# Kernel tuning notes

Measured on AMD Instinct MI355X. Metric: run time of the kernel, lower is better.

Reference implementation:

```python
import jax, jax.numpy as jnp
import numpy as np

E, T, D_IN, D_H = 8, 2048, 2048, 5632


def setup_inputs() -> dict:
    key = jax.random.key(0)
    kx, kg, kd, ku = jax.random.split(key, 4)
    scale = 0.02  # init_std-like scaling for weights
    return {
        "x": jax.random.normal(kx, (E, T, D_IN), dtype=jnp.float32),
        "gate_proj": jax.random.normal(kg, (E, D_IN, D_H), dtype=jnp.float32) * scale,
        "down_proj": jax.random.normal(kd, (E, D_IN, D_H), dtype=jnp.float32) * scale,
        "up_proj": jax.random.normal(ku, (E, D_H, D_IN), dtype=jnp.float32) * scale,
        "tokens_per_expert": T,
    }


def reference(x, gate_proj, down_proj, up_proj, tokens_per_expert):
    # ep_size=1: dispatch/combine are identity. Grouped SwiGLU per expert.
    # x: [E, T, d_in]; gate/down: [E, d_in, d_h]; up: [E, d_h, d_in]
    g = jnp.einsum('etd,edh->eth', x, gate_proj)
    u = jnp.einsum('etd,edh->eth', x, down_proj)
    h = jax.nn.silu(g) * u  # [E, T, d_h]
    out = jnp.einsum('eth,ehd->etd', h, up_proj)  # [E, T, d_in]
    return out
```

## Files before the change

### kernel.cpp

```cpp
#include <hip/hip_runtime.h>
#include <hip/hip_bf16.h>


#define NEXP 8
#define TT   2048
#define DIN  2048
#define DH   5632
#define KP   2080

using short8 = __attribute__((ext_vector_type(8))) short;
using f32x4  = __attribute__((ext_vector_type(4))) float;

static __device__ __forceinline__ unsigned short f2bf(float f) {
    unsigned int i = __float_as_uint(f);
    return (unsigned short)((i + 0x7FFFu + ((i >> 16) & 1u)) >> 16);
}
static __device__ __forceinline__ void gld16(const void* g, void* l) {
    __builtin_amdgcn_global_load_lds(
        (const __attribute__((address_space(1))) void*)g,
        (__attribute__((address_space(3))) void*)l, 16, 0, 0);
}

__global__ __launch_bounds__(512, 2) void gemm_gu(
    const unsigned short* __restrict__ Xb,
    const unsigned short* __restrict__ Wgt,
    const unsigned short* __restrict__ Wdt,
    unsigned short* __restrict__ Hb)
{
    __shared__ __align__(16) unsigned short lds[81920];

    const int tid  = threadIdx.x;
    const int wave = tid >> 6, lane = tid & 63;
    const int l15 = lane & 15, l4 = lane >> 4;
    const int wr = wave >> 2, wc = wave & 3;

    const int bid = blockIdx.x;
    const int e   = bid & 7;
    const int cu  = bid >> 3;
    const int m0  = (cu & 7) * 256;
    const int nb  = cu >> 3;

    const unsigned short* Ae = Xb + (size_t)e * TT * KP;
    unsigned short* He = Hb + (size_t)e * TT * DH;

    const int c0 = tid, c1 = 512 + tid;
    const int cs0 = c0 ^ ((c0 >> 3) & 7), cs1 = c1 ^ ((c1 >> 3) & 7);
    const int row0 = cs0 >> 3, col0 = (cs0 & 7) * 8;
    const int row1 = cs1 >> 3, col1 = (cs1 & 7) * 8;

    int ibA[4][2], ibB[2][2];
#pragma unroll
    for (int s = 0; s < 4; ++s)
#pragma unroll
        for (int ks = 0; ks < 2; ++ks) {
            const int r = wr * 64 + s * 16 + l15;
            ibA[s][ks] = (r * 128 + ks * 64 + l4 * 16) ^ ((r & 7) << 4);
        }
#pragma unroll
    for (int s = 0; s < 2; ++s)
#pragma unroll
        for (int ks = 0; ks < 2; ++ks) {
            const int r = wc * 32 + s * 16 + l15;
            ibB[s][ks] = (r * 128 + ks * 64 + l4 * 16) ^ ((r & 7) << 4);
        }

    f32x4 acc[8][4] = {};
    short8 Aq[4][2], Gq[2][2], Dq[2][2];

    char* ldsb = (char*)lds;
    auto stageA = [&](int ro, int kk, int so) {
        gld16(Ae + (size_t)(m0 + ro + row0) * KP + (kk + col0), ldsb + so + wave * 1024);
        gld16(Ae + (size_t)(m0 + ro + row1) * KP + (kk + col1), ldsb + so + 8192 + wave * 1024);
    };
    auto stageW = [&](const unsigned short* p, int kk, int so) {
        gld16(p + (size_t)row0 * KP + (kk + col0), ldsb + so + wave * 1024);
        gld16(p + (size_t)row1 * KP + (kk + col1), ldsb + so + 8192 + wave * 1024);
    };
    auto w10 = [](int x) { return x >= 10 ? x - 10 : x; };

    const size_t NSTEP = (size_t)512 * KP;
    const unsigned short* Gc = Wgt + (size_t)e * DH * KP + (size_t)(nb * 128) * KP;
    const unsigned short* Dc = Wdt + (size_t)e * DH * KP + (size_t)(nb * 128) * KP;

    stageA(0, 0, 0 << 14);  stageW(Gc, 0, 1 << 14);  stageW(Dc, 0, 2 << 14);  stageA(128, 0, 3 << 14);
    stageA(0, 64, 4 << 14); stageW(Gc, 64, 5 << 14); stageW(Dc, 64, 6 << 14);
    asm volatile("s_waitcnt vmcnt(6)" ::: "memory");
    asm volatile("s_barrier" ::: "memory");

    const char* ldsc = (const char*)lds;
    int q = 0;
    for (int i = 0; i < 11; ++i) {
        const unsigned short* Gn = Gc + NSTEP;
        const unsigned short* Dn = Dc + NSTEP;
        for (int t = 0; t < 32; ++t) {
            const int g = (i << 5) + t;
            const int sA0 = q << 14;
            const int sG  = w10(q + 1) << 14;
            const int sD  = w10(q + 2) << 14;
            const int sA1 = w10(q + 3) << 14;
            const int stA1 = w10(q + 7) << 14;
            const int stA0 = w10(q + 8) << 14;
            const int stG  = w10(q + 9) << 14;
            const int stD  = sA0;

#pragma unroll
            for (int s = 0; s < 4; ++s) {
                Aq[s][0] = *(const short8*)(ldsc + sA0 + ibA[s][0]);
                Aq[s][1] = *(const short8*)(ldsc + sA0 + ibA[s][1]);
            }
#pragma unroll
            for (int s = 0; s < 2; ++s) {
                Gq[s][0] = *(const short8*)(ldsc + sG + ibB[s][0]);
                Gq[s][1] = *(const short8*)(ldsc + sG + ibB[s][1]);
                Dq[s][0] = *(const short8*)(ldsc + sD + ibB[s][0]);
                Dq[s][1] = *(const short8*)(ldsc + sD + ibB[s][1]);
            }
            if (i < 10 || t + 1 < 32)
                stageA(128, ((t + 1) & 31) * 64, stA1);
            asm volatile("s_waitcnt lgkmcnt(0)" ::: "memory");
            __builtin_amdgcn_sched_barrier(0);
            __builtin_amdgcn_s_setprio(1);
#pragma unroll
            for (int m = 0; m < 4; ++m)
#pragma unroll
                for (int n = 0; n < 2; ++n) {
                    acc[m][n] = __builtin_amdgcn_mfma_f32_16x16x32_bf16(Aq[m][0], Gq[n][0], acc[m][n], 0, 0, 0);
                    acc[m][n] = __builtin_amdgcn_mfma_f32_16x16x32_bf16(Aq[m][1], Gq[n][1], acc[m][n], 0, 0, 0);
                }
            __builtin_amdgcn_s_setprio(0);
            if (i < 10 || t + 2 < 32)
                stageA(0, ((t + 2) & 31) * 64, stA0);
            __builtin_amdgcn_s_setprio(1);
#pragma unroll
            for (int m = 0; m < 4; ++m)
#pragma unroll
                for (int n = 0; n < 2; ++n) {
                    acc[m][2 + n] = __builtin_amdgcn_mfma_f32_16x16x32_bf16(Aq[m][0], Dq[n][0], acc[m][2 + n], 0, 0, 0);
                    acc[m][2 + n] = __builtin_amdgcn_mfma_f32_16x16x32_bf16(Aq[m][1], Dq[n][1], acc[m][2 + n], 0, 0, 0);
                }
            __builtin_amdgcn_s_setprio(0);
#pragma unroll
            for (int s = 0; s < 4; ++s) {
                Aq[s][0] = *(const short8*)(ldsc + sA1 + ibA[s][0]);
                Aq[s][1] = *(const short8*)(ldsc + sA1 + ibA[s][1]);
            }
            if (i < 10 || t + 2 < 32)
                stageW((t + 2 < 32) ? Gc : Gn, ((t + 2) & 31) * 64, stG);
            asm volatile("s_waitcnt lgkmcnt(0)" ::: "memory");
            __builtin_amdgcn_sched_barrier(0);
            __builtin_amdgcn_s_setprio(1);
#pragma unroll
            for (int m = 0; m < 4; ++m)
#pragma unroll
                for (int n = 0; n < 2; ++n) {
                    acc[4 + m][2 + n] = __builtin_amdgcn_mfma_f32_16x16x32_bf16(Aq[m][0], Dq[n][0], acc[4 + m][2 + n], 0, 0, 0);
                    acc[4 + m][2 + n] = __builtin_amdgcn_mfma_f32_16x16x32_bf16(Aq[m][1], Dq[n][1], acc[4 + m][2 + n], 0, 0, 0);
                }
#pragma unroll
            for (int m = 0; m < 4; ++m)
#pragma unroll
                for (int n = 0; n < 2; ++n) {
                    acc[4 + m][n] = __builtin_amdgcn_mfma_f32_16x16x32_bf16(Aq[m][0], Gq[n][0], acc[4 + m][n], 0, 0, 0);
                    acc[4 + m][n] = __builtin_amdgcn_mfma_f32_16x16x32_bf16(Aq[m][1], Gq[n][1], acc[4 + m][n], 0, 0, 0);
                }
            __builtin_amdgcn_s_setprio(0);
            asm volatile("s_barrier" ::: "memory");
            if (i < 10 || t + 2 < 32)
                stageW((t + 2 < 32) ? Dc : Dn, ((t + 2) & 31) * 64, stD);
            if (g < 350)       asm volatile("s_waitcnt vmcnt(6)" ::: "memory");
            else if (g == 350) asm volatile("s_waitcnt vmcnt(0)" ::: "memory");
            asm volatile("s_barrier" ::: "memory");
            q = w10(q + 4);
        }

        const int n0i = (4 * i + nb) * 128;
#pragma unroll
        for (int fm = 0; fm < 8; ++fm) {
            const int row_b = m0 + (fm >> 2) * 128 + wr * 64 + (fm & 3) * 16 + l4 * 4;
#pragma unroll
            for (int nr = 0; nr < 2; ++nr) {
                const int col = n0i + wc * 32 + nr * 16 + l15;
#pragma unroll
                for (int j = 0; j < 4; ++j) {
                    const float gv = acc[fm][nr][j];
                    const float uv = acc[fm][2 + nr][j];
                    const float h = gv / (1.f + __expf(-gv)) * uv;
                    He[(size_t)(row_b + j) * DH + col] = f2bf(h);
                }
            }
        }
#pragma unroll
        for (int m = 0; m < 8; ++m)
#pragma unroll
            for (int n = 0; n < 4; ++n)
                acc[m][n] = (f32x4){0.f, 0.f, 0.f, 0.f};
        Gc = Gn; Dc = Dn;
    }
}

__global__ __launch_bounds__(512, 2) void gemm_out(
    const unsigned short* __restrict__ Ab,
    const unsigned short* __restrict__ Btb,
    float* __restrict__ Cf)
{
    __shared__ __align__(16) unsigned short lds[81920];

    const int tid  = threadIdx.x;
    const int wave = tid >> 6, lane = tid & 63;
    const int l15 = lane & 15, l4 = lane >> 4;
    const int wr = wave >> 2, wc = wave & 3;

    const int bid = blockIdx.x;
    const int e   = bid & 7;
    const int cu  = bid >> 3;
    const int m0  = (cu & 7) * 256;
    const int nb  = cu >> 3;

    const int N = DIN, K = DH;
    const unsigned short* Ae = Ab + (size_t)e * TT * DH;

    const int c0 = tid, c1 = 512 + tid;
    const int cs0 = c0 ^ ((c0 >> 3) & 7), cs1 = c1 ^ ((c1 >> 3) & 7);
    const int row0 = cs0 >> 3, col0 = (cs0 & 7) * 8;
    const int row1 = cs1 >> 3, col1 = (cs1 & 7) * 8;

    int ibA[4][2], ibB[2][2];
#pragma unroll
    for (int s = 0; s < 4; ++s)
#pragma unroll
        for (int ks = 0; ks < 2; ++ks) {
            const int r = wr * 64 + s * 16 + l15;
            ibA[s][ks] = (r * 128 + ks * 64 + l4 * 16) ^ ((r & 7) << 4);
        }
#pragma unroll
    for (int s = 0; s < 2; ++s)
#pragma unroll
        for (int ks = 0; ks < 2; ++ks) {
            const int r = wc * 32 + s * 16 + l15;
            ibB[s][ks] = (r * 128 + ks * 64 + l4 * 16) ^ ((r & 7) << 4);
        }

    f32x4 acc[8][4] = {};
    short8 Aq[4][2], B0q[2][2], B1q[2][2];

    char* ldsb = (char*)lds;
    auto stageA = [&](int ro, int kk, int so) {
        gld16(Ae + (size_t)(m0 + ro + row0) * K + (kk + col0), ldsb + so + wave * 1024);
        gld16(Ae + (size_t)(m0 + ro + row1) * K + (kk + col1), ldsb + so + 8192 + wave * 1024);
    };
    auto stageB = [&](const unsigned short* base, int co, int kk, int so) {
        gld16(base + (size_t)(co + row0) * K + (kk + col0), ldsb + so + wave * 1024);
        gld16(base + (size_t)(co + row1) * K + (kk + col1), ldsb + so + 8192 + wave * 1024);
    };
    auto w10 = [](int x) { return x >= 10 ? x - 10 : x; };

    const size_t NSTEP = (size_t)1024 * K;
    const unsigned short* Bc = Btb + (size_t)e * DIN * DH + (size_t)(nb * 256) * K;

    stageA(0, 0, 0 << 14); stageB(Bc, 0, 0, 1 << 14); stageB(Bc, 128, 0, 2 << 14); stageA(128, 0, 3 << 14);
    stageA(0, 64, 4 << 14); stageB(Bc, 0, 64, 5 << 14); stageB(Bc, 128, 64, 6 << 14);
    asm volatile("s_waitcnt vmcnt(6)" ::: "memory");
    asm volatile("s_barrier" ::: "memory");

    const char* ldsc = (const char*)lds;
    int q = 0;
    for (int i = 0; i < 2; ++i) {
        const unsigned short* Bn = Bc + NSTEP;
        for (int t = 0; t < 88; ++t) {
            const int g = i * 88 + t;
            const int sA0 = q << 14;
            const int sB0 = w10(q + 1) << 14;
            const int sB1 = w10(q + 2) << 14;
            const int sA1 = w10(q + 3) << 14;
            const int stA1 = w10(q + 7) << 14;
            const int stA0 = w10(q + 8) << 14;
            const int stB0 = w10(q + 9) << 14;
            const int stB1 = sA0;

#pragma unroll
            for (int s = 0; s < 4; ++s) {
                Aq[s][0] = *(const short8*)(ldsc + sA0 + ibA[s][0]);
                Aq[s][1] = *(const short8*)(ldsc + sA0 + ibA[s][1]);
            }
#pragma unroll
            for (int s = 0; s < 2; ++s) {
                B0q[s][0] = *(const short8*)(ldsc + sB0 + ibB[s][0]);
                B0q[s][1] = *(const short8*)(ldsc + sB0 + ibB[s][1]);
                B1q[s][0] = *(const short8*)(ldsc + sB1 + ibB[s][0]);
                B1q[s][1] = *(const short8*)(ldsc + sB1 + ibB[s][1]);
            }
            {
                const int tt = t + 1;
                if (i < 1 || tt < 88)
                    stageA(128, (tt >= 88 ? tt - 88 : tt) * 64, stA1);
            }
            asm volatile("s_waitcnt lgkmcnt(0)" ::: "memory");
            __builtin_amdgcn_sched_barrier(0);
            __builtin_amdgcn_s_setprio(1);
#pragma unroll
            for (int m = 0; m < 4; ++m)
#pragma unroll
                for (int n = 0; n < 2; ++n) {
                    acc[m][n] = __builtin_amdgcn_mfma_f32_16x16x32_bf16(Aq[m][0], B0q[n][0], acc[m][n], 0, 0, 0);
                    acc[m][n] = __builtin_amdgcn_mfma_f32_16x16x32_bf16(Aq[m][1], B0q[n][1], acc[m][n], 0, 0, 0);
                }
            __builtin_amdgcn_s_setprio(0);
            {
                const int tt = t + 2;
                if (i < 1 || tt < 88)
                    stageA(0, (tt >= 88 ? tt - 88 : tt) * 64, stA0);
            }
            __builtin_amdgcn_s_setprio(1);
#pragma unroll
            for (int m = 0; m < 4; ++m)
#pragma unroll
                for (int n = 0; n < 2; ++n) {
                    acc[m][2 + n] = __builtin_amdgcn_mfma_f32_16x16x32_bf16(Aq[m][0], B1q[n][0], acc[m][2 + n], 0, 0, 0);
                    acc[m][2 + n] = __builtin_amdgcn_mfma_f32_16x16x32_bf16(Aq[m][1], B1q[n][1], acc[m][2 + n], 0, 0, 0);
                }
            __builtin_amdgcn_s_setprio(0);
#pragma unroll
            for (int s = 0; s < 4; ++s) {
                Aq[s][0] = *(const short8*)(ldsc + sA1 + ibA[s][0]);
                Aq[s][1] = *(const short8*)(ldsc + sA1 + ibA[s][1]);
            }
            {
                const int tt = t + 2;
                if (i < 1 || tt < 88)
                    stageB((tt >= 88 ? Bn : Bc), 0, (tt >= 88 ? tt - 88 : tt) * 64, stB0);
            }
            asm volatile("s_waitcnt lgkmcnt(0)" ::: "memory");
            __builtin_amdgcn_sched_barrier(0);
            __builtin_amdgcn_s_setprio(1);
#pragma unroll
            for (int m = 0; m < 4; ++m)
#pragma unroll
                for (int n = 0; n < 2; ++n) {
                    acc[4 + m][2 + n] = __builtin_amdgcn_mfma_f32_16x16x32_bf16(Aq[m][0], B1q[n][0], acc[4 + m][2 + n], 0, 0, 0);
                    acc[4 + m][2 + n] = __builtin_amdgcn_mfma_f32_16x16x32_bf16(Aq[m][1], B1q[n][1], acc[4 + m][2 + n], 0, 0, 0);
                }
#pragma unroll
            for (int m = 0; m < 4; ++m)
#pragma unroll
                for (int n = 0; n < 2; ++n) {
                    acc[4 + m][n] = __builtin_amdgcn_mfma_f32_16x16x32_bf16(Aq[m][0], B0q[n][0], acc[4 + m][n], 0, 0, 0);
                    acc[4 + m][n] = __builtin_amdgcn_mfma_f32_16x16x32_bf16(Aq[m][1], B0q[n][1], acc[4 + m][n], 0, 0, 0);
                }
            __builtin_amdgcn_s_setprio(0);
            asm volatile("s_barrier" ::: "memory");
            {
                const int tt = t + 2;
                if (i < 1 || tt < 88)
                    stageB((tt >= 88 ? Bn : Bc), 128, (tt >= 88 ? tt - 88 : tt) * 64, stB1);
            }
            if (g < 174)       asm volatile("s_waitcnt vmcnt(6)" ::: "memory");
            else if (g == 174) asm volatile("s_waitcnt vmcnt(0)" ::: "memory");
            asm volatile("s_barrier" ::: "memory");
            q = w10(q + 4);
        }

        const int n0i = (4 * i + nb) * 256;
        float* Ce = Cf + (size_t)e * TT * DIN;
#pragma unroll
        for (int fm = 0; fm < 8; ++fm) {
            const int row_b = (fm >> 2) * 128 + wr * 64 + (fm & 3) * 16 + l4 * 4;
#pragma unroll
            for (int fn = 0; fn < 4; ++fn) {
                const int col = n0i + (fn >> 1) * 128 + wc * 32 + (fn & 1) * 16 + l15;
#pragma unroll
                for (int j = 0; j < 4; ++j)
                    Ce[(size_t)(m0 + row_b + j) * N + col] = acc[fm][fn][j];
            }
        }
#pragma unroll
        for (int m = 0; m < 8; ++m)
#pragma unroll
            for (int n = 0; n < 4; ++n)
                acc[m][n] = (f32x4){0.f, 0.f, 0.f, 0.f};
        Bc = Bn;
    }
}

__global__ __launch_bounds__(256) void transpose_f32_bf16(
    const float* __restrict__ in, unsigned short* __restrict__ out,
    int R, int C, int opitch, size_t ies, size_t oes)
{
    in  += (size_t)blockIdx.z * ies;
    out += (size_t)blockIdx.z * oes;
    __shared__ unsigned short t[64][65];
    const int tid = threadIdx.x;
    const int lr = tid >> 4, lc = (tid & 15) * 4;
    const int r0 = blockIdx.y * 64, c0 = blockIdx.x * 64;
#pragma unroll
    for (int i = 0; i < 4; ++i) {
        const int row = lr + i * 16;
        const float4 v = *(const float4*)(in + (size_t)(r0 + row) * C + c0 + lc);
        t[row][lc + 0] = f2bf(v.x); t[row][lc + 1] = f2bf(v.y);
        t[row][lc + 2] = f2bf(v.z); t[row][lc + 3] = f2bf(v.w);
    }
    __syncthreads();
#pragma unroll
    for (int i = 0; i < 4; ++i) {
        const int crow = lr + i * 16;
        ushort4 wv;
        wv.x = t[lc + 0][crow]; wv.y = t[lc + 1][crow];
        wv.z = t[lc + 2][crow]; wv.w = t[lc + 3][crow];
        *(ushort4*)(out + (size_t)(c0 + crow) * opitch + r0 + lc) = wv;
    }
}

__global__ __launch_bounds__(256) void conv_pad_f32_bf16(
    const float* __restrict__ in, unsigned short* __restrict__ out, int n8)
{
    int i = blockIdx.x * 256 + threadIdx.x;
    const int stride = gridDim.x * 256;
    for (; i < n8; i += stride) {
        const int row = i >> 8;
        const int col = (i & 255) * 8;
        const float4 v0 = *(const float4*)(in + (size_t)row * DIN + col);
        const float4 v1 = *(const float4*)(in + (size_t)row * DIN + col + 4);
        ushort4 a, b;
        a.x = f2bf(v0.x); a.y = f2bf(v0.y); a.z = f2bf(v0.z); a.w = f2bf(v0.w);
        b.x = f2bf(v1.x); b.y = f2bf(v1.y); b.z = f2bf(v1.z); b.w = f2bf(v1.w);
        *(ushort4*)(out + (size_t)row * KP + col) = a;
        *(ushort4*)(out + (size_t)row * KP + col + 4) = b;
    }
}

extern "C" void kernel_launch(void* const* d_in, const int* in_sizes, int n_in,
                              void* d_out, int out_size, void* d_ws, size_t ws_size,
                              hipStream_t stream)
{
    const float* x  = (const float*)d_in[0];
    const float* wg = (const float*)d_in[1];
    const float* wd = (const float*)d_in[2];
    const float* wu = (const float*)d_in[3];
    float* out = (float*)d_out;

    const size_t XSZ = (size_t)TT * KP;
    const size_t WPSZ = (size_t)DH * KP;
    const size_t WSZ = (size_t)DIN * DH;
    unsigned short* xb  = (unsigned short*)d_ws;
    unsigned short* wgt = xb  + (size_t)NEXP * XSZ;
    unsigned short* wdt = wgt + (size_t)NEXP * WPSZ;
    unsigned short* hb  = wdt + (size_t)NEXP * WPSZ;

    conv_pad_f32_bf16<<<4096, 256, 0, stream>>>(x, xb, NEXP * TT * (DIN / 8));
    transpose_f32_bf16<<<dim3(DH / 64, DIN / 64, NEXP), 256, 0, stream>>>(
        wg, wgt, DIN, DH, KP, WSZ, WPSZ);
    transpose_f32_bf16<<<dim3(DH / 64, DIN / 64, NEXP), 256, 0, stream>>>(
        wd, wdt, DIN, DH, KP, WSZ, WPSZ);
    gemm_gu<<<256, 512, 0, stream>>>(xb, wgt, wdt, hb);
    transpose_f32_bf16<<<dim3(DIN / 64, DH / 64, NEXP), 256, 0, stream>>>(
        wu, wgt, DH, DIN, DH, WSZ, WSZ);
    gemm_out<<<256, 512, 0, stream>>>(hb, wgt, out);
}
```

Before: 1.324 ms.

## Replace rotating 10-slot LDS ring with fixed double-buffered slots and unrolled steps

```diff
diff --git a/kernel.cpp b/kernel.cpp
--- a/kernel.cpp
+++ b/kernel.cpp
@@ -20,6 +20,86 @@
         (const __attribute__((address_space(1))) void*)g,
         (__attribute__((address_space(3))) void*)l, 16, 0, 0);
 }
+
+#define GU_STEP(TCONST, SA0B, SA1B, SSA1B, SSA0B, GB, DB)                      \
+  {                                                                            \
+    const int t = (TCONST);                                                    \
+    const int g = (i << 5) + t;                                                \
+    _Pragma("unroll")                                                          \
+    for (int s = 0; s < 4; ++s) {                                              \
+      Aq[s][0] = *(const short8*)(ldsc + (SA0B) + ibA[s][0]);                  \
+      Aq[s][1] = *(const short8*)(ldsc + (SA0B) + ibA[s][1]);                  \
+    }                                                                          \
+    _Pragma("unroll")                                                          \
+    for (int s = 0; s < 2; ++s) {                                              \
+      Gq[s][0] = *(const short8*)(ldsc + (GB) + ibBG[s][0]);                   \
+      Gq[s][1] = *(const short8*)(ldsc + (GB) + ibBG[s][1]);                   \
+      Dq[s][0] = *(const short8*)(ldsc + (DB) + ibBD[s][0]);                   \
+      Dq[s][1] = *(const short8*)(ldsc + (DB) + ibBD[s][1]);                   \
+    }                                                                          \
+    if (i < 10 || t < 31) {                                                    \
+      const unsigned short* ps = Ae128 + ((t + 1) & 31) * 64;                  \
+      gld16(ps + loffA0, ldsb + (SSA1B) + wvoff);                              \
+      gld16(ps + loffA1, ldsb + (SSA1B) + 8192 + wvoff);                       \
+    }                                                                          \
+    asm volatile("s_waitcnt lgkmcnt(0)" ::: "memory");                         \
+    __builtin_amdgcn_sched_barrier(0);                                         \
+    __builtin_amdgcn_s_setprio(1);                                             \
+    _Pragma("unroll")                                                          \
+    for (int m = 0; m < 4; ++m)                                                \
+      _Pragma("unroll")                                                        \
+      for (int n = 0; n < 2; ++n) {                                            \
+        acc[m][n] = __builtin_amdgcn_mfma_f32_16x16x32_bf16(Aq[m][0], Gq[n][0], acc[m][n], 0, 0, 0); \
+        acc[m][n] = __builtin_amdgcn_mfma_f32_16x16x32_bf16(Aq[m][1], Gq[n][1], acc[m][n], 0, 0, 0); \
+      }                                                                        \
+    _Pragma("unroll")                                                          \
+    for (int m = 0; m < 4; ++m)                                                \
+      _Pragma("unroll")                                                        \
+      for (int n = 0; n < 2; ++n) {                                            \
+        acc[m][2 + n] = __builtin_amdgcn_mfma_f32_16x16x32_bf16(Aq[m][0], Dq[n][0], acc[m][2 + n], 0, 0, 0); \
+        acc[m][2 + n] = __builtin_amdgcn_mfma_f32_16x16x32_bf16(Aq[m][1], Dq[n][1], acc[m][2 + n], 0, 0, 0); \
+      }                                                                        \
+    __builtin_amdgcn_s_setprio(0);                                             \
+    _Pragma("unroll")                                                          \
+    for (int s = 0; s < 4; ++s) {                                              \
+      Aq[s][0] = *(const short8*)(ldsc + (SA1B) + ibA[s][0]);                  \
+      Aq[s][1] = *(const short8*)(ldsc + (SA1B) + ibA[s][1]);                  \
+    }                                                                          \
+    asm volatile("s_waitcnt lgkmcnt(0)" ::: "memory");                         \
+    __builtin_amdgcn_sched_barrier(0);                                         \
+    __builtin_amdgcn_s_setprio(1);                                             \
+    _Pragma("unroll")                                                          \
+    for (int m = 0; m < 4; ++m)                                                \
+      _Pragma("unroll")                                                        \
+      for (int n = 0; n < 2; ++n) {                                            \
+        acc[4 + m][2 + n] = __builtin_amdgcn_mfma_f32_16x16x32_bf16(Aq[m][0], Dq[n][0], acc[4 + m][2 + n], 0, 0, 0); \
+        acc[4 + m][2 + n] = __builtin_amdgcn_mfma_f32_16x16x32_bf16(Aq[m][1], Dq[n][1], acc[4 + m][2 + n], 0, 0, 0); \
+      }                                                                        \
+    _Pragma("unroll")                                                          \
+    for (int m = 0; m < 4; ++m)                                                \
+      _Pragma("unroll")                                                        \
+      for (int n = 0; n < 2; ++n) {                                            \
+        acc[4 + m][n] = __builtin_amdgcn_mfma_f32_16x16x32_bf16(Aq[m][0], Gq[n][0], acc[4 + m][n], 0, 0, 0); \
+        acc[4 + m][n] = __builtin_amdgcn_mfma_f32_16x16x32_bf16(Aq[m][1], Gq[n][1], acc[4 + m][n], 0, 0, 0); \
+      }                                                                        \
+    __builtin_amdgcn_s_setprio(0);                                             \
+    asm volatile("s_barrier" ::: "memory");                                    \
+    if (i < 10 || t < 30) {                                                    \
+      const int k2 = ((t + 2) & 31) * 64;                                      \
+      const unsigned short* pa = Ae + k2;                                      \
+      gld16(pa + loffA0, ldsb + (SSA0B) + wvoff);                              \
+      gld16(pa + loffA1, ldsb + (SSA0B) + 8192 + wvoff);                       \
+      const unsigned short* pg = ((t < 30) ? Gc : Gn) + k2;                    \
+      gld16(pg + loffW0, ldsb + 65536 + (GB) + wvoff);                         \
+      gld16(pg + loffW1, ldsb + 65536 + (GB) + 8192 + wvoff);                  \
+      const unsigned short* pd = ((t < 30) ? Dc : Dn) + k2;                    \
+      gld16(pd + loffW0, ldsb + 98304 + (DB) + wvoff);                         \
+      gld16(pd + loffW1, ldsb + 98304 + (DB) + 8192 + wvoff);                  \
+    }                                                                          \
+    if (g < 350)       asm volatile("s_waitcnt vmcnt(6)" ::: "memory");        \
+    else if (g == 350) asm volatile("s_waitcnt vmcnt(0)" ::: "memory");        \
+    asm volatile("s_barrier" ::: "memory");                                    \
+  }
 
 __global__ __launch_bounds__(512, 2) void gemm_gu(
     const unsigned short* __restrict__ Xb,
@@ -27,7 +107,7 @@
     const unsigned short* __restrict__ Wdt,
     unsigned short* __restrict__ Hb)
 {
-    __shared__ __align__(16) unsigned short lds[81920];
+    __shared__ __align__(16) unsigned short lds[65536];
 
     const int tid  = threadIdx.x;
     const int wave = tid >> 6, lane = tid & 63;
@@ -40,15 +120,20 @@
     const int m0  = (cu & 7) * 256;
     const int nb  = cu >> 3;
 
-    const unsigned short* Ae = Xb + (size_t)e * TT * KP;
+    const unsigned short* Ae = Xb + (size_t)e * TT * KP + (size_t)m0 * KP;
+    const unsigned short* Ae128 = Ae + (size_t)128 * KP;
     unsigned short* He = Hb + (size_t)e * TT * DH;
 
     const int c0 = tid, c1 = 512 + tid;
     const int cs0 = c0 ^ ((c0 >> 3) & 7), cs1 = c1 ^ ((c1 >> 3) & 7);
     const int row0 = cs0 >> 3, col0 = (cs0 & 7) * 8;
     const int row1 = cs1 >> 3, col1 = (cs1 & 7) * 8;
-
-    int ibA[4][2], ibB[2][2];
+    const size_t loffA0 = (size_t)row0 * KP + col0;
+    const size_t loffA1 = (size_t)row1 * KP + col1;
+    const size_t loffW0 = loffA0, loffW1 = loffA1;
+    const int wvoff = wave * 1024;
+
+    int ibA[4][2], ibBG[2][2], ibBD[2][2];
 #pragma unroll
     for (int s = 0; s < 4; ++s)
 #pragma unroll
@@ -61,116 +146,44 @@
 #pragma unroll
         for (int ks = 0; ks < 2; ++ks) {
             const int r = wc * 32 + s * 16 + l15;
-            ibB[s][ks] = (r * 128 + ks * 64 + l4 * 16) ^ ((r & 7) << 4);
+            const int b = (r * 128 + ks * 64 + l4 * 16) ^ ((r & 7) << 4);
+            ibBG[s][ks] = b + 65536;
+            ibBD[s][ks] = b + 98304;
         }
 
     f32x4 acc[8][4] = {};
     short8 Aq[4][2], Gq[2][2], Dq[2][2];
 
     char* ldsb = (char*)lds;
-    auto stageA = [&](int ro, int kk, int so) {
-        gld16(Ae + (size_t)(m0 + ro + row0) * KP + (kk + col0), ldsb + so + wave * 1024);
-        gld16(Ae + (size_t)(m0 + ro + row1) * KP + (kk + col1), ldsb + so + 8192 + wave * 1024);
-    };
-    auto stageW = [&](const unsigned short* p, int kk, int so) {
-        gld16(p + (size_t)row0 * KP + (kk + col0), ldsb + so + wave * 1024);
-        gld16(p + (size_t)row1 * KP + (kk + col1), ldsb + so + 8192 + wave * 1024);
-    };
-    auto w10 = [](int x) { return x >= 10 ? x - 10 : x; };
+    const char* ldsc = (const char*)lds;
 
     const size_t NSTEP = (size_t)512 * KP;
     const unsigned short* Gc = Wgt + (size_t)e * DH * KP + (size_t)(nb * 128) * KP;
     const unsigned short* Dc = Wdt + (size_t)e * DH * KP + (size_t)(nb * 128) * KP;
 
-    stageA(0, 0, 0 << 14);  stageW(Gc, 0, 1 << 14);  stageW(Dc, 0, 2 << 14);  stageA(128, 0, 3 << 14);
-    stageA(0, 64, 4 << 14); stageW(Gc, 64, 5 << 14); stageW(Dc, 64, 6 << 14);
+    gld16(Ae    + loffA0, ldsb + 0 + wvoff);
+    gld16(Ae    + loffA1, ldsb + 0 + 8192 + wvoff);
+    gld16(Ae128 + loffA0, ldsb + 16384 + wvoff);
+    gld16(Ae128 + loffA1, ldsb + 16384 + 8192 + wvoff);
+    gld16(Gc    + loffW0, ldsb + 65536 + wvoff);
+    gld16(Gc    + loffW1, ldsb + 65536 + 8192 + wvoff);
+    gld16(Dc    + loffW0, ldsb + 98304 + wvoff);
+    gld16(Dc    + loffW1, ldsb + 98304 + 8192 + wvoff);
+    gld16(Ae + 64 + loffA0, ldsb + 32768 + wvoff);
+    gld16(Ae + 64 + loffA1, ldsb + 32768 + 8192 + wvoff);
+    gld16(Gc + 64 + loffW0, ldsb + 65536 + 16384 + wvoff);
+    gld16(Gc + 64 + loffW1, ldsb + 65536 + 16384 + 8192 + wvoff);
+    gld16(Dc + 64 + loffW0, ldsb + 98304 + 16384 + wvoff);
+    gld16(Dc + 64 + loffW1, ldsb + 98304 + 16384 + 8192 + wvoff);
     asm volatile("s_waitcnt vmcnt(6)" ::: "memory");
     asm volatile("s_barrier" ::: "memory");
 
-    const char* ldsc = (const char*)lds;
-    int q = 0;
     for (int i = 0; i < 11; ++i) {
         const unsigned short* Gn = Gc + NSTEP;
         const unsigned short* Dn = Dc + NSTEP;
-        for (int t = 0; t < 32; ++t) {
-            const int g = (i << 5) + t;
-            const int sA0 = q << 14;
-            const int sG  = w10(q + 1) << 14;
-            const int sD  = w10(q + 2) << 14;
-            const int sA1 = w10(q + 3) << 14;
-            const int stA1 = w10(q + 7) << 14;
-            const int stA0 = w10(q + 8) << 14;
-            const int stG  = w10(q + 9) << 14;
-            const int stD  = sA0;
-
-#pragma unroll
-            for (int s = 0; s < 4; ++s) {
-                Aq[s][0] = *(const short8*)(ldsc + sA0 + ibA[s][0]);
-                Aq[s][1] = *(const short8*)(ldsc + sA0 + ibA[s][1]);
-            }
-#pragma unroll
-            for (int s = 0; s < 2; ++s) {
-                Gq[s][0] = *(const short8*)(ldsc + sG + ibB[s][0]);
-                Gq[s][1] = *(const short8*)(ldsc + sG + ibB[s][1]);
-                Dq[s][0] = *(const short8*)(ldsc + sD + ibB[s][0]);
-                Dq[s][1] = *(const short8*)(ldsc + sD + ibB[s][1]);
-            }
-            if (i < 10 || t + 1 < 32)
-                stageA(128, ((t + 1) & 31) * 64, stA1);
-            asm volatile("s_waitcnt lgkmcnt(0)" ::: "memory");
-            __builtin_amdgcn_sched_barrier(0);
-            __builtin_amdgcn_s_setprio(1);
-#pragma unroll
-            for (int m = 0; m < 4; ++m)
-#pragma unroll
-                for (int n = 0; n < 2; ++n) {
-                    acc[m][n] = __builtin_amdgcn_mfma_f32_16x16x32_bf16(Aq[m][0], Gq[n][0], acc[m][n], 0, 0, 0);
-                    acc[m][n] = __builtin_amdgcn_mfma_f32_16x16x32_bf16(Aq[m][1], Gq[n][1], acc[m][n], 0, 0, 0);
-                }
-            __builtin_amdgcn_s_setprio(0);
-            if (i < 10 || t + 2 < 32)
-                stageA(0, ((t + 2) & 31) * 64, stA0);
-            __builtin_amdgcn_s_setprio(1);
-#pragma unroll
-            for (int m = 0; m < 4; ++m)
-#pragma unroll
-                for (int n = 0; n < 2; ++n) {
-                    acc[m][2 + n] = __builtin_amdgcn_mfma_f32_16x16x32_bf16(Aq[m][0], Dq[n][0], acc[m][2 + n], 0, 0, 0);
-                    acc[m][2 + n] = __builtin_amdgcn_mfma_f32_16x16x32_bf16(Aq[m][1], Dq[n][1], acc[m][2 + n], 0, 0, 0);
-                }
-            __builtin_amdgcn_s_setprio(0);
-#pragma unroll
-            for (int s = 0; s < 4; ++s) {
-                Aq[s][0] = *(const short8*)(ldsc + sA1 + ibA[s][0]);
-                Aq[s][1] = *(const short8*)(ldsc + sA1 + ibA[s][1]);
-            }
-            if (i < 10 || t + 2 < 32)
-                stageW((t + 2 < 32) ? Gc : Gn, ((t + 2) & 31) * 64, stG);
-            asm volatile("s_waitcnt lgkmcnt(0)" ::: "memory");
-            __builtin_amdgcn_sched_barrier(0);
-            __builtin_amdgcn_s_setprio(1);
-#pragma unroll
-            for (int m = 0; m < 4; ++m)
-#pragma unroll
-                for (int n = 0; n < 2; ++n) {
-                    acc[4 + m][2 + n] = __builtin_amdgcn_mfma_f32_16x16x32_bf16(Aq[m][0], Dq[n][0], acc[4 + m][2 + n], 0, 0, 0);
-                    acc[4 + m][2 + n] = __builtin_amdgcn_mfma_f32_16x16x32_bf16(Aq[m][1], Dq[n][1], acc[4 + m][2 + n], 0, 0, 0);
-                }
-#pragma unroll
-            for (int m = 0; m < 4; ++m)
-#pragma unroll
-                for (int n = 0; n < 2; ++n) {
-                    acc[4 + m][n] = __builtin_amdgcn_mfma_f32_16x16x32_bf16(Aq[m][0], Gq[n][0], acc[4 + m][n], 0, 0, 0);
-                    acc[4 + m][n] = __builtin_amdgcn_mfma_f32_16x16x32_bf16(Aq[m][1], Gq[n][1], acc[4 + m][n], 0, 0, 0);
-                }
-            __builtin_amdgcn_s_setprio(0);
-            asm volatile("s_barrier" ::: "memory");
-            if (i < 10 || t + 2 < 32)
-                stageW((t + 2 < 32) ? Dc : Dn, ((t + 2) & 31) * 64, stD);
-            if (g < 350)       asm volatile("s_waitcnt vmcnt(6)" ::: "memory");
-            else if (g == 350) asm volatile("s_waitcnt vmcnt(0)" ::: "memory");
-            asm volatile("s_barrier" ::: "memory");
-            q = w10(q + 4);
+        for (int t2 = 0; t2 < 16; ++t2) {
+            GU_STEP(2 * t2,     0,     16384, 49152, 0,     0,     0)
+            GU_STEP(2 * t2 + 1, 32768, 49152, 16384, 32768, 16384, 16384)
         }
 
         const int n0i = (4 * i + nb) * 128;
@@ -198,12 +211,93 @@
     }
 }
 
+#define OUT_STEP(TCONST, SA0B, SA1B, SSA1B, SSA0B, B0B, B1B)                   \
+  {                                                                            \
+    const int t = (TCONST);                                                    \
+    const int g = i * 88 + t;                                                  \
+    _Pragma("unroll")                                                          \
+    for (int s = 0; s < 4; ++s) {                                              \
+      Aq[s][0] = *(const short8*)(ldsc + (SA0B) + ibA[s][0]);                  \
+      Aq[s][1] = *(const short8*)(ldsc + (SA0B) + ibA[s][1]);                  \
+    }                                                                          \
+    _Pragma("unroll")                                                          \
+    for (int s = 0; s < 2; ++s) {                                              \
+      B0q[s][0] = *(const short8*)(ldsc + (B0B) + ibB0[s][0]);                 \
+      B0q[s][1] = *(const short8*)(ldsc + (B0B) + ibB0[s][1]);                 \
+      B1q[s][0] = *(const short8*)(ldsc + (B1B) + ibB1[s][0]);                 \
+      B1q[s][1] = *(const short8*)(ldsc + (B1B) + ibB1[s][1]);                 \
+    }                                                                          \
+    if (i < 1 || t < 87) {                                                     \
+      const int k1 = ((t + 1 >= 88) ? (t + 1 - 88) : (t + 1)) * 64;            \
+      const unsigned short* ps = Ae128 + k1;                                   \
+      gld16(ps + loffA0, ldsb + (SSA1B) + wvoff);                              \
+      gld16(ps + loffA1, ldsb + (SSA1B) + 8192 + wvoff);                       \
+    }                                                                          \
+    asm volatile("s_waitcnt lgkmcnt(0)" ::: "memory");                         \
+    __builtin_amdgcn_sched_barrier(0);                                         \
+    __builtin_amdgcn_s_setprio(1);                                             \
+    _Pragma("unroll")                                                          \
+    for (int m = 0; m < 4; ++m)                                                \
+      _Pragma("unroll")                                                        \
+      for (int n = 0; n < 2; ++n) {                                            \
+        acc[m][n] = __builtin_amdgcn_mfma_f32_16x16x32_bf16(Aq[m][0], B0q[n][0], acc[m][n], 0, 0, 0); \
+        acc[m][n] = __builtin_amdgcn_mfma_f32_16x16x32_bf16(Aq[m][1], B0q[n][1], acc[m][n], 0, 0, 0); \
+      }                                                                        \
+    _Pragma("unroll")                                                          \
+    for (int m = 0; m < 4; ++m)                                                \
+      _Pragma("unroll")                                                        \
+      for (int n = 0; n < 2; ++n) {                                            \
+        acc[m][2 + n] = __builtin_amdgcn_mfma_f32_16x16x32_bf16(Aq[m][0], B1q[n][0], acc[m][2 + n], 0, 0, 0); \
+        acc[m][2 + n] = __builtin_amdgcn_mfma_f32_16x16x32_bf16(Aq[m][1], B1q[n][1], acc[m][2 + n], 0, 0, 0); \
+      }                                                                        \
+    __builtin_amdgcn_s_setprio(0);                                             \
+    _Pragma("unroll")                                                          \
+    for (int s = 0; s < 4; ++s) {                                              \
+      Aq[s][0] = *(const short8*)(ldsc + (SA1B) + ibA[s][0]);                  \
+      Aq[s][1] = *(const short8*)(ldsc + (SA1B) + ibA[s][1]);                  \
+    }                                                                          \
+    asm volatile("s_waitcnt lgkmcnt(0)" ::: "memory");                         \
+    __builtin_amdgcn_sched_barrier(0);                                         \
+    __builtin_amdgcn_s_setprio(1);                                             \
+    _Pragma("unroll")                                                          \
+    for (int m = 0; m < 4; ++m)                                                \
+      _Pragma("unroll")                                                        \
+      for (int n = 0; n < 2; ++n) {                                            \
+        acc[4 + m][2 + n] = __builtin_amdgcn_mfma_f32_16x16x32_bf16(Aq[m][0], B1q[n][0], acc[4 + m][2 + n], 0, 0, 0); \
+        acc[4 + m][2 + n] = __builtin_amdgcn_mfma_f32_16x16x32_bf16(Aq[m][1], B1q[n][1], acc[4 + m][2 + n], 0, 0, 0); \
+      }                                                                        \
+    _Pragma("unroll")                                                          \
+    for (int m = 0; m < 4; ++m)                                                \
+      _Pragma("unroll")                                                        \
+      for (int n = 0; n < 2; ++n) {                                            \
+        acc[4 + m][n] = __builtin_amdgcn_mfma_f32_16x16x32_bf16(Aq[m][0], B0q[n][0], acc[4 + m][n], 0, 0, 0); \
+        acc[4 + m][n] = __builtin_amdgcn_mfma_f32_16x16x32_bf16(Aq[m][1], B0q[n][1], acc[4 + m][n], 0, 0, 0); \
+      }                                                                        \
+    __builtin_amdgcn_s_setprio(0);                                             \
+    asm volatile("s_barrier" ::: "memory");                                    \
+    if (i < 1 || t < 86) {                                                     \
+      const int k2 = ((t + 2 >= 88) ? (t + 2 - 88) : (t + 2)) * 64;            \
+      const unsigned short* pa = Ae + k2;                                      \
+      gld16(pa + loffA0, ldsb + (SSA0B) + wvoff);                              \
+      gld16(pa + loffA1, ldsb + (SSA0B) + 8192 + wvoff);                       \
+      const unsigned short* pb = ((t < 86) ? Bc : Bn) + k2;                    \
+      gld16(pb + loffB0, ldsb + 65536 + (B0B) + wvoff);                        \
+      gld16(pb + loffB1, ldsb + 65536 + (B0B) + 8192 + wvoff);                 \
+      const unsigned short* pc = pb + (size_t)128 * DH;                        \
+      gld16(pc + loffB0, ldsb + 98304 + (B1B) + wvoff);                        \
+      gld16(pc + loffB1, ldsb + 98304 + (B1B) + 8192 + wvoff);                 \
+    }                                                                          \
+    if (g < 174)       asm volatile("s_waitcnt vmcnt(6)" ::: "memory");        \
+    else if (g == 174) asm volatile("s_waitcnt vmcnt(0)" ::: "memory");        \
+    asm volatile("s_barrier" ::: "memory");                                    \
+  }
+
 __global__ __launch_bounds__(512, 2) void gemm_out(
     const unsigned short* __restrict__ Ab,
     const unsigned short* __restrict__ Btb,
     float* __restrict__ Cf)
 {
-    __shared__ __align__(16) unsigned short lds[81920];
+    __shared__ __align__(16) unsigned short lds[65536];
 
     const int tid  = threadIdx.x;
     const int wave = tid >> 6, lane = tid & 63;
@@ -216,15 +310,19 @@
     const int m0  = (cu & 7) * 256;
     const int nb  = cu >> 3;
 
-    const int N = DIN, K = DH;
-    const unsigned short* Ae = Ab + (size_t)e * TT * DH;
+    const unsigned short* Ae = Ab + (size_t)e * TT * DH + (size_t)m0 * DH;
+    const unsigned short* Ae128 = Ae + (size_t)128 * DH;
 
     const int c0 = tid, c1 = 512 + tid;
     const int cs0 = c0 ^ ((c0 >> 3) & 7), cs1 = c1 ^ ((c1 >> 3) & 7);
     const int row0 = cs0 >> 3, col0 = (cs0 & 7) * 8;
     const int row1 = cs1 >> 3, col1 = (cs1 & 7) * 8;
-
-    int ibA[4][2], ibB[2][2];
+    const size_t loffA0 = (size_t)row0 * DH + col0;
+    const size_t loffA1 = (size_t)row1 * DH + col1;
+    const size_t loffB0 = loffA0, loffB1 = loffA1;
+    const int wvoff = wave * 1024;
+
+    int ibA[4][2], ibB0[2][2], ibB1[2][2];
 #pragma unroll
     for (int s = 0; s < 4; ++s)
 #pragma unroll
@@ -237,126 +335,42 @@
 #pragma unroll
         for (int ks = 0; ks < 2; ++ks) {
             const int r = wc * 32 + s * 16 + l15;
-            ibB[s][ks] = (r * 128 + ks * 64 + l4 * 16) ^ ((r & 7) << 4);
+            const int b = (r * 128 + ks * 64 + l4 * 16) ^ ((r & 7) << 4);
+            ibB0[s][ks] = b + 65536;
+            ibB1[s][ks] = b + 98304;
         }
 
     f32x4 acc[8][4] = {};
     short8 Aq[4][2], B0q[2][2], B1q[2][2];
 
     char* ldsb = (char*)lds;
-    auto stageA = [&](int ro, int kk, int so) {
-        gld16(Ae + (size_t)(m0 + ro + row0) * K + (kk + col0), ldsb + so + wave * 1024);
-        gld16(Ae + (size_t)(m0 + ro + row1) * K + (kk + col1), ldsb + so + 8192 + wave * 1024);
-    };
-    auto stageB = [&](const unsigned short* base, int co, int kk, int so) {
-        gld16(base + (size_t)(co + row0) * K + (kk + col0), ldsb + so + wave * 1024);
-        gld16(base + (size_t)(co + row1) * K + (kk + col1), ldsb + so + 8192 + wave * 1024);
-    };
-    auto w10 = [](int x) { return x >= 10 ? x - 10 : x; };
-
-    const size_t NSTEP = (size_t)1024 * K;
-    const unsigned short* Bc = Btb + (size_t)e * DIN * DH + (size_t)(nb * 256) * K;
-
-    stageA(0, 0, 0 << 14); stageB(Bc, 0, 0, 1 << 14); stageB(Bc, 128, 0, 2 << 14); stageA(128, 0, 3 << 14);
-    stageA(0, 64, 4 << 14); stageB(Bc, 0, 64, 5 << 14); stageB(Bc, 128, 64, 6 << 14);
+    const char* ldsc = (const char*)lds;
+
+    const size_t NSTEP = (size_t)1024 * DH;
+    const unsigned short* Bc = Btb + (size_t)e * DIN * DH + (size_t)(nb * 256) * DH;
+
+    gld16(Ae    + loffA0, ldsb + 0 + wvoff);
+    gld16(Ae    + loffA1, ldsb + 0 + 8192 + wvoff);
+    gld16(Ae128 + loffA0, ldsb + 16384 + wvoff);
+    gld16(Ae128 + loffA1, ldsb + 16384 + 8192 + wvoff);
+    gld16(Bc    + loffB0, ldsb + 65536 + wvoff);
+    gld16(Bc    + loffB1, ldsb + 65536 + 8192 + wvoff);
+    gld16(Bc + (size_t)128 * DH + loffB0, ldsb + 98304 + wvoff);
+    gld16(Bc + (size_t)128 * DH + loffB1, ldsb + 98304 + 8192 + wvoff);
+    gld16(Ae + 64 + loffA0, ldsb + 32768 + wvoff);
+    gld16(Ae + 64 + loffA1, ldsb + 32768 + 8192 + wvoff);
+    gld16(Bc + 64 + loffB0, ldsb + 65536 + 16384 + wvoff);
+    gld16(Bc + 64 + loffB1, ldsb + 65536 + 16384 + 8192 + wvoff);
+    gld16(Bc + (size_t)128 * DH + 64 + loffB0, ldsb + 98304 + 16384 + wvoff);
+    gld16(Bc + (size_t)128 * DH + 64 + loffB1, ldsb + 98304 + 16384 + 8192 + wvoff);
     asm volatile("s_waitcnt vmcnt(6)" ::: "memory");
     asm volatile("s_barrier" ::: "memory");
 
-    const char* ldsc = (const char*)lds;
-    int q = 0;
     for (int i = 0; i < 2; ++i) {
         const unsigned short* Bn = Bc + NSTEP;
-        for (int t = 0; t < 88; ++t) {
-            const int g = i * 88 + t;
-            const int sA0 = q << 14;
-            const int sB0 = w10(q + 1) << 14;
-            const int sB1 = w10(q + 2) << 14;
-            const int sA1 = w10(q + 3) << 14;
-            const int stA1 = w10(q + 7) << 14;
-            const int stA0 = w10(q + 8) << 14;
-            const int stB0 = w10(q + 9) << 14;
-            const int stB1 = sA0;
-
-#pragma unroll
-            for (int s = 0; s < 4; ++s) {
-                Aq[s][0] = *(const short8*)(ldsc + sA0 + ibA[s][0]);
-                Aq[s][1] = *(const short8*)(ldsc + sA0 + ibA[s][1]);
-            }
-#pragma unroll
-            for (int s = 0; s < 2; ++s) {
-                B0q[s][0] = *(const short8*)(ldsc + sB0 + ibB[s][0]);
-                B0q[s][1] = *(const short8*)(ldsc + sB0 + ibB[s][1]);
-                B1q[s][0] = *(const short8*)(ldsc + sB1 + ibB[s][0]);
-                B1q[s][1] = *(const short8*)(ldsc + sB1 + ibB[s][1]);
-            }
-            {
-                const int tt = t + 1;
-                if (i < 1 || tt < 88)
-                    stageA(128, (tt >= 88 ? tt - 88 : tt) * 64, stA1);
-            }
-            asm volatile("s_waitcnt lgkmcnt(0)" ::: "memory");
-            __builtin_amdgcn_sched_barrier(0);
-            __builtin_amdgcn_s_setprio(1);
-#pragma unroll
-            for (int m = 0; m < 4; ++m)
-#pragma unroll
-                for (int n = 0; n < 2; ++n) {
-                    acc[m][n] = __builtin_amdgcn_mfma_f32_16x16x32_bf16(Aq[m][0], B0q[n][0], acc[m][n], 0, 0, 0);
-                    acc[m][n] = __builtin_amdgcn_mfma_f32_16x16x32_bf16(Aq[m][1], B0q[n][1], acc[m][n], 0, 0, 0);
-                }
-            __builtin_amdgcn_s_setprio(0);
-            {
-                const int tt = t + 2;
-                if (i < 1 || tt < 88)
-                    stageA(0, (tt >= 88 ? tt - 88 : tt) * 64, stA0);
-            }
-            __builtin_amdgcn_s_setprio(1);
-#pragma unroll
-            for (int m = 0; m < 4; ++m)
-#pragma unroll
-                for (int n = 0; n < 2; ++n) {
-                    acc[m][2 + n] = __builtin_amdgcn_mfma_f32_16x16x32_bf16(Aq[m][0], B1q[n][0], acc[m][2 + n], 0, 0, 0);
-                    acc[m][2 + n] = __builtin_amdgcn_mfma_f32_16x16x32_bf16(Aq[m][1], B1q[n][1], acc[m][2 + n], 0, 0, 0);
-                }
-            __builtin_amdgcn_s_setprio(0);
-#pragma unroll
-            for (int s = 0; s < 4; ++s) {
-                Aq[s][0] = *(const short8*)(ldsc + sA1 + ibA[s][0]);
-                Aq[s][1] = *(const short8*)(ldsc + sA1 + ibA[s][1]);
-            }
-            {
-                const int tt = t + 2;
-                if (i < 1 || tt < 88)
-                    stageB((tt >= 88 ? Bn : Bc), 0, (tt >= 88 ? tt - 88 : tt) * 64, stB0);
-            }
-            asm volatile("s_waitcnt lgkmcnt(0)" ::: "memory");
-            __builtin_amdgcn_sched_barrier(0);
-            __builtin_amdgcn_s_setprio(1);
-#pragma unroll
-            for (int m = 0; m < 4; ++m)
-#pragma unroll
-                for (int n = 0; n < 2; ++n) {
-                    acc[4 + m][2 + n] = __builtin_amdgcn_mfma_f32_16x16x32_bf16(Aq[m][0], B1q[n][0], acc[4 + m][2 + n], 0, 0, 0);
-                    acc[4 + m][2 + n] = __builtin_amdgcn_mfma_f32_16x16x32_bf16(Aq[m][1], B1q[n][1], acc[4 + m][2 + n], 0, 0, 0);
-                }
-#pragma unroll
-            for (int m = 0; m < 4; ++m)
-#pragma unroll
-                for (int n = 0; n < 2; ++n) {
-                    acc[4 + m][n] = __builtin_amdgcn_mfma_f32_16x16x32_bf16(Aq[m][0], B0q[n][0], acc[4 + m][n], 0, 0, 0);
-                    acc[4 + m][n] = __builtin_amdgcn_mfma_f32_16x16x32_bf16(Aq[m][1], B0q[n][1], acc[4 + m][n], 0, 0, 0);
-                }
-            __builtin_amdgcn_s_setprio(0);
-            asm volatile("s_barrier" ::: "memory");
-            {
-                const int tt = t + 2;
-                if (i < 1 || tt < 88)
-                    stageB((tt >= 88 ? Bn : Bc), 128, (tt >= 88 ? tt - 88 : tt) * 64, stB1);
-            }
-            if (g < 174)       asm volatile("s_waitcnt vmcnt(6)" ::: "memory");
-            else if (g == 174) asm volatile("s_waitcnt vmcnt(0)" ::: "memory");
-            asm volatile("s_barrier" ::: "memory");
-            q = w10(q + 4);
+        for (int t2 = 0; t2 < 44; ++t2) {
+            OUT_STEP(2 * t2,     0,     16384, 49152, 0,     0,     0)
+            OUT_STEP(2 * t2 + 1, 32768, 49152, 16384, 32768, 16384, 16384)
         }
 
         const int n0i = (4 * i + nb) * 256;
@@ -369,7 +383,7 @@
                 const int col = n0i + (fn >> 1) * 128 + wc * 32 + (fn & 1) * 16 + l15;
 #pragma unroll
                 for (int j = 0; j < 4; ++j)
-                    Ce[(size_t)(m0 + row_b + j) * N + col] = acc[fm][fn][j];
+                    Ce[(size_t)(m0 + row_b + j) * DIN + col] = acc[fm][fn][j];
             }
         }
 #pragma unroll
```

New measurement: 1.533 ms. +15.7%, slower.
